# Performance work log

Measured on AMD Instinct MI355X. Metric: run time of the kernel, lower is better.

Reference implementation:

```python
import jax, jax.numpy as jnp
import numpy as np

DIM = 1024
INTER = 512
E = 16            # n_routed_experts
TOPK = 4          # n_activated_experts
N_GROUPS = 4
TOPK_GROUPS = 2
ROUTE_SCALE = 1.0
INIT_STD = 0.02
B, S = 2, 1024


def setup_inputs() -> dict:
    key = jax.random.key(0)
    ks = jax.random.split(key, 8)
    return {
        "x": jax.random.normal(ks[0], (B, S, DIM), jnp.float32),
        "gate_w": jax.random.normal(ks[1], (E, DIM), jnp.float32) * INIT_STD,
        "gate_bias": jnp.zeros((E,), jnp.float32),
        "w1": jax.random.normal(ks[2], (E, INTER, DIM), jnp.float32) * INIT_STD,
        "w2": jax.random.normal(ks[3], (E, DIM, INTER), jnp.float32) * INIT_STD,
        "w3": jax.random.normal(ks[4], (E, INTER, DIM), jnp.float32) * INIT_STD,
        "ws1": jax.random.normal(ks[5], (INTER, DIM), jnp.float32) * INIT_STD,
        "ws2": jax.random.normal(ks[6], (DIM, INTER), jnp.float32) * INIT_STD,
        "ws3": jax.random.normal(ks[7], (INTER, DIM), jnp.float32) * INIT_STD,
    }


def reference(x, gate_w, gate_bias, w1, w2, w3, ws1, ws2, ws3):
    Bx, Sx, D = x.shape
    T = Bx * Sx
    xf = x.reshape(T, D)

    # ---- Gate: sigmoid scores + expert bias, group-limited top-k ----
    scores = jax.nn.sigmoid(xf @ gate_w.T)          # [T, E]
    original_scores = scores
    s = scores + gate_bias                          # bias only affects selection
    sg = s.reshape(T, N_GROUPS, E // N_GROUPS)
    group_scores = sg.max(axis=-1)                  # [T, G]
    _, gidx = jax.lax.top_k(group_scores, TOPK_GROUPS)
    keep = jnp.zeros((T, N_GROUPS), bool).at[jnp.arange(T)[:, None], gidx].set(True)
    s_masked = jnp.where(keep[:, :, None], sg, -jnp.inf).reshape(T, E)
    _, idx = jax.lax.top_k(s_masked, TOPK)          # [T, topk]
    weights = jnp.take_along_axis(original_scores, idx, axis=1) * ROUTE_SCALE

    # combine weights as sparse [T, E] matrix (scatter of top-k weights)
    comb = jnp.zeros((T, E), x.dtype).at[jnp.arange(T)[:, None], idx].add(weights)

    # ---- Routed experts: SwiGLU per expert, weighted combine ----
    h1 = jnp.einsum('td,eid->tei', xf, w1)          # [T, E, inter]
    h3 = jnp.einsum('td,eid->tei', xf, w3)
    h = jax.nn.silu(h1) * h3
    y = jnp.einsum('tei,edi,te->td', h, w2, comb)   # weighted combine

    # ---- Shared expert (SwiGLU MLP) ----
    z = (jax.nn.silu(xf @ ws1.T) * (xf @ ws3.T)) @ ws2.T

    return (y + z).reshape(Bx, Sx, D)
```

## Files before the change

### kernel.cpp

```cpp
#include <hip/hip_runtime.h>

#define T_TOK  2048
#define DIMD   1024
#define INTERI 512
#define NEXP   16
#define NSEG   17

typedef __bf16 bf16x8 __attribute__((ext_vector_type(8)));
typedef float  f32x4  __attribute__((ext_vector_type(4)));

__device__ __forceinline__ unsigned short f2b(float f) {
    union { float f; unsigned int u; } c; c.f = f;
    unsigned int u = c.u;
    unsigned int r = (u + 0x7FFFu + ((u >> 16) & 1u)) >> 16;
    return (unsigned short)r;
}

__device__ __forceinline__ void cp16(const unsigned short* g, unsigned short* l) {
    __builtin_amdgcn_global_load_lds(
        (const __attribute__((address_space(1))) unsigned int*)g,
        (__attribute__((address_space(3))) unsigned int*)l,
        16, 0, 0);
}

__global__ __launch_bounds__(256) void cvt_all_kernel(
    const float* __restrict__ x,  const float* __restrict__ w1,
    const float* __restrict__ w3, const float* __restrict__ w2,
    const float* __restrict__ ws1, const float* __restrict__ ws3,
    const float* __restrict__ ws2,
    unsigned short* __restrict__ xb,  unsigned short* __restrict__ w1b,
    unsigned short* __restrict__ w3b, unsigned short* __restrict__ w2b,
    unsigned short* __restrict__ ws1b, unsigned short* __restrict__ ws3b,
    unsigned short* __restrict__ ws2b)
{
    int g = blockIdx.x * 256 + threadIdx.x;
    const float* s; unsigned short* d; int i;
    if      (g < 524288)  { s = x;   d = xb;   i = g; }
    else if (g < 2621440) { s = w1;  d = w1b;  i = g - 524288; }
    else if (g < 4718592) { s = w3;  d = w3b;  i = g - 2621440; }
    else if (g < 6815744) { s = w2;  d = w2b;  i = g - 4718592; }
    else if (g < 6946816) { s = ws1; d = ws1b; i = g - 6815744; }
    else if (g < 7077888) { s = ws3; d = ws3b; i = g - 6946816; }
    else                  { s = ws2; d = ws2b; i = g - 7077888; }
    float4 v = ((const float4*)s)[i];
    ushort4 o;
    o.x = f2b(v.x); o.y = f2b(v.y); o.z = f2b(v.z); o.w = f2b(v.w);
    ((ushort4*)d)[i] = o;
}

__global__ __launch_bounds__(256) void gate_score_kernel(
    const float* __restrict__ x, const float* __restrict__ gw,
    const float* __restrict__ gb,
    unsigned* __restrict__ sel, float4* __restrict__ selw)
{
    int tok  = blockIdx.x * 4 + (threadIdx.x >> 6);
    int lane = threadIdx.x & 63;
    const float* xp = x + (size_t)tok * DIMD;
    float xv[16];
#pragma unroll
    for (int j = 0; j < 16; ++j) xv[j] = xp[j * 64 + lane];

    float sc[16];
#pragma unroll
    for (int e = 0; e < 16; ++e) {
        const float* gwe = gw + e * DIMD;
        float p0 = 0.f, p1 = 0.f;
#pragma unroll
        for (int j = 0; j < 16; j += 2) {
            p0 += xv[j]     * gwe[j * 64 + lane];
            p1 += xv[j + 1] * gwe[(j + 1) * 64 + lane];
        }
        float p = p0 + p1;
#pragma unroll
        for (int o = 32; o; o >>= 1) p += __shfl_xor(p, o, 64);
        sc[e] = p;
    }
    if (lane != 0) return;

    float orig[16], s[16];
#pragma unroll
    for (int e = 0; e < 16; ++e) {
        orig[e] = 1.f / (1.f + expf(-sc[e]));
        s[e] = orig[e] + gb[e];
    }
    float gmax[4];
#pragma unroll
    for (int g = 0; g < 4; ++g) {
        float m = s[4 * g];
        for (int j = 1; j < 4; ++j) m = fmaxf(m, s[4 * g + j]);
        gmax[g] = m;
    }
    int g0 = 0;
    for (int g = 1; g < 4; ++g) if (gmax[g] > gmax[g0]) g0 = g;
    int g1 = -1;
    for (int g = 0; g < 4; ++g) { if (g == g0) continue; if (g1 < 0 || gmax[g] > gmax[g1]) g1 = g; }
    unsigned keep = (0xFu << (4 * g0)) | (0xFu << (4 * g1));
    unsigned used = 0;
    unsigned pk = 0;
    float w4[4];
    for (int j = 0; j < 4; ++j) {
        int best = -1;
        for (int e = 0; e < 16; ++e) {
            if (!((keep >> e) & 1u) || ((used >> e) & 1u)) continue;
            if (best < 0 || s[e] > s[best]) best = e;
        }
        used |= 1u << best;
        pk |= ((unsigned)best) << (4 * j);
        w4[j] = orig[best];
    }
    sel[tok] = pk;
    selw[tok] = make_float4(w4[0], w4[1], w4[2], w4[3]);
}

__global__ __launch_bounds__(256) void build_lists_kernel(
    const unsigned* __restrict__ sel, const float4* __restrict__ selw,
    int* __restrict__ counts, int* __restrict__ lst, float* __restrict__ lstw)
{
    const int e    = blockIdx.x;
    const int tid  = threadIdx.x;
    const int wave = tid >> 6;
    const int lane = tid & 63;

    __shared__ int wsum[4];
    __shared__ int basev;
    if (tid == 0) basev = 0;
    __syncthreads();

    for (int c = 0; c < T_TOK / 256; ++c) {
        int t = c * 256 + tid;
        unsigned s = sel[t];
        int match = -1;
#pragma unroll
        for (int j = 0; j < 4; ++j)
            if (((s >> (4 * j)) & 15u) == (unsigned)e) match = j;
        unsigned long long m = __ballot(match >= 0);
        int wpre = __popcll(m & ((1ull << lane) - 1ull));
        if (lane == 0) wsum[wave] = __popcll(m);
        __syncthreads();
        int pre = basev;
        for (int wv = 0; wv < wave; ++wv) pre += wsum[wv];
        if (match >= 0) {
            int pos = pre + wpre;
            lst [e * T_TOK + pos] = t | (match << 16);
            const float* wp = (const float*)&selw[t];
            lstw[e * T_TOK + pos] = wp[match];
        }
        __syncthreads();
        if (tid == 0) basev += wsum[0] + wsum[1] + wsum[2] + wsum[3];
        __syncthreads();
    }
    if (tid == 0) counts[e] = basev;
}

__global__ __launch_bounds__(256, 4) void gemm1_kernel(
    const unsigned short* __restrict__ xb,
    const unsigned short* __restrict__ w1b,
    const unsigned short* __restrict__ w3b,
    const unsigned short* __restrict__ ws1b,
    const unsigned short* __restrict__ ws3b,
    const int* __restrict__ counts,
    const int* __restrict__ lst,
    unsigned short* __restrict__ H)
{
    int b = blockIdx.x;
    int seg, mt, nt;
    if (b < 2048) {
        int xcd = b & 7, slot = b >> 3;
        seg = xcd + 8 * (slot >> 7);
        int tile = slot & 127;
        nt = tile & 3; mt = tile >> 2;
    } else {
        seg = NEXP;
        int tile = b - 2048;
        nt = tile & 3; mt = tile >> 2;
    }
    const int n_e = (seg == NEXP) ? T_TOK : counts[seg];
    const int m0  = mt * 64;
    if (m0 >= n_e) return;
    const int n0  = nt * 128;

    const unsigned short* w1p = (seg == NEXP) ? ws1b : w1b + (size_t)seg * INTERI * DIMD;
    const unsigned short* w3p = (seg == NEXP) ? ws3b : w3b + (size_t)seg * INTERI * DIMD;
    const int* lste = lst + seg * T_TOK;

    __shared__ __align__(16) unsigned short lA [2][64][32];
    __shared__ __align__(16) unsigned short lB1[2][128][32];
    __shared__ __align__(16) unsigned short lB3[2][128][32];

    const int tid  = threadIdx.x;
    const int wave = tid >> 6;
    const int lane = tid & 63;
    const int r4   = tid >> 2;
    const int skg  = (tid & 3) * 8;

    int ra = m0 + r4; if (ra > n_e - 1) ra = n_e - 1;
    int tok = (seg == NEXP) ? ra : (lste[ra] & 0xFFFF);
    const unsigned short* gA  = xb  + (size_t)tok * DIMD + skg;
    const unsigned short* gB1a = w1p + (size_t)(n0 + r4) * DIMD + skg;
    const unsigned short* gB1b = w1p + (size_t)(n0 + r4 + 64) * DIMD + skg;
    const unsigned short* gB3a = w3p + (size_t)(n0 + r4) * DIMD + skg;
    const unsigned short* gB3b = w3p + (size_t)(n0 + r4 + 64) * DIMD + skg;

    const int wb = wave * 512;

    f32x4 acc1[2][4], acc3[2][4];
    const f32x4 zero = {0.f, 0.f, 0.f, 0.f};
#pragma unroll
    for (int i = 0; i < 2; ++i)
#pragma unroll
        for (int j = 0; j < 4; ++j) { acc1[i][j] = zero; acc3[i][j] = zero; }

    const int wm   = (wave & 1) * 32;
    const int wn   = (wave >> 1) * 64;
    const int quad = lane >> 4;
    const int lrow = lane & 15;

    for (int k0 = 0; k0 < DIMD; k0 += 64) {
#pragma unroll
        for (int kk = 0; kk < 2; ++kk) {
            cp16(gA   + k0 + kk * 32, &lA [kk][0][0]  + wb);
            cp16(gB1a + k0 + kk * 32, &lB1[kk][0][0]  + wb);
            cp16(gB1b + k0 + kk * 32, &lB1[kk][64][0] + wb);
            cp16(gB3a + k0 + kk * 32, &lB3[kk][0][0]  + wb);
            cp16(gB3b + k0 + kk * 32, &lB3[kk][64][0] + wb);
        }
        __syncthreads();
#pragma unroll
        for (int kk = 0; kk < 2; ++kk) {
            bf16x8 a[2], b1[4], b3[4];
#pragma unroll
            for (int t = 0; t < 2; ++t)
                a[t] = *(const bf16x8*)&lA[kk][wm + t * 16 + lrow][quad * 8];
#pragma unroll
            for (int t = 0; t < 4; ++t) {
                b1[t] = *(const bf16x8*)&lB1[kk][wn + t * 16 + lrow][quad * 8];
                b3[t] = *(const bf16x8*)&lB3[kk][wn + t * 16 + lrow][quad * 8];
            }
#pragma unroll
            for (int i = 0; i < 2; ++i)
#pragma unroll
                for (int j = 0; j < 4; ++j) {
                    acc1[i][j] = __builtin_amdgcn_mfma_f32_16x16x32_bf16(a[i], b1[j], acc1[i][j], 0, 0, 0);
                    acc3[i][j] = __builtin_amdgcn_mfma_f32_16x16x32_bf16(a[i], b3[j], acc3[i][j], 0, 0, 0);
                }
        }
        __syncthreads();
    }

    unsigned short* Hseg = H + (size_t)seg * T_TOK * INTERI;
#pragma unroll
    for (int i = 0; i < 2; ++i) {
        int rbase = m0 + wm + i * 16 + quad * 4;
#pragma unroll
        for (int r = 0; r < 4; ++r) {
            int row = rbase + r;
            if (row >= n_e) continue;
            unsigned short* hrow = Hseg + (size_t)row * INTERI + n0 + wn + lrow;
#pragma unroll
            for (int j = 0; j < 4; ++j) {
                float v1 = acc1[i][j][r];
                float v3 = acc3[i][j][r];
                float hv = (v1 / (1.f + __expf(-v1))) * v3;
                hrow[j * 16] = f2b(hv);
            }
        }
    }
}

__global__ __launch_bounds__(256, 4) void gemm2_kernel(
    const unsigned short* __restrict__ H,
    const unsigned short* __restrict__ w2b,
    const unsigned short* __restrict__ ws2b,
    const int* __restrict__ counts,
    const int* __restrict__ lst,
    const float* __restrict__ lstw,
    float* __restrict__ P)
{
    int b = blockIdx.x;
    int seg, mt, nt;
    if (b < 4096) {
        int xcd = b & 7, slot = b >> 3;
        seg = xcd + 8 * (slot >> 8);
        int tile = slot & 255;
        nt = tile & 7; mt = tile >> 3;
    } else {
        seg = NEXP;
        int tile = b - 4096;
        nt = tile & 7; mt = tile >> 3;
    }
    const int n_e = (seg == NEXP) ? T_TOK : counts[seg];
    const int m0  = mt * 64;
    if (m0 >= n_e) return;
    const int n0  = nt * 128;

    const unsigned short* w2p  = (seg == NEXP) ? ws2b : w2b + (size_t)seg * DIMD * INTERI;
    const unsigned short* Hseg = H + (size_t)seg * T_TOK * INTERI;

    __shared__ __align__(16) unsigned short lA[2][64][32];
    __shared__ __align__(16) unsigned short lB[2][128][32];

    const int tid  = threadIdx.x;
    const int wave = tid >> 6;
    const int lane = tid & 63;
    const int r4   = tid >> 2;
    const int skg  = (tid & 3) * 8;

    int ra = m0 + r4; if (ra > n_e - 1) ra = n_e - 1;
    const unsigned short* gA  = Hseg + (size_t)ra * INTERI + skg;
    const unsigned short* gB0 = w2p + (size_t)(n0 + r4) * INTERI + skg;
    const unsigned short* gB1 = w2p + (size_t)(n0 + r4 + 64) * INTERI + skg;

    const int wb = wave * 512;

    f32x4 acc[2][4];
    const f32x4 zero = {0.f, 0.f, 0.f, 0.f};
#pragma unroll
    for (int i = 0; i < 2; ++i)
#pragma unroll
        for (int j = 0; j < 4; ++j) acc[i][j] = zero;

    const int wm   = (wave & 1) * 32;
    const int wn   = (wave >> 1) * 64;
    const int quad = lane >> 4;
    const int lrow = lane & 15;

    for (int k0 = 0; k0 < INTERI; k0 += 64) {
#pragma unroll
        for (int kk = 0; kk < 2; ++kk) {
            cp16(gA  + k0 + kk * 32, &lA[kk][0][0]  + wb);
            cp16(gB0 + k0 + kk * 32, &lB[kk][0][0]  + wb);
            cp16(gB1 + k0 + kk * 32, &lB[kk][64][0] + wb);
        }
        __syncthreads();
#pragma unroll
        for (int kk = 0; kk < 2; ++kk) {
            bf16x8 a[2], bv[4];
#pragma unroll
            for (int t = 0; t < 2; ++t)
                a[t] = *(const bf16x8*)&lA[kk][wm + t * 16 + lrow][quad * 8];
#pragma unroll
            for (int t = 0; t < 4; ++t)
                bv[t] = *(const bf16x8*)&lB[kk][wn + t * 16 + lrow][quad * 8];
#pragma unroll
            for (int i = 0; i < 2; ++i)
#pragma unroll
                for (int j = 0; j < 4; ++j)
                    acc[i][j] = __builtin_amdgcn_mfma_f32_16x16x32_bf16(a[i], bv[j], acc[i][j], 0, 0, 0);
        }
        __syncthreads();
    }

#pragma unroll
    for (int i = 0; i < 2; ++i) {
        int rbase = m0 + wm + i * 16 + quad * 4;
#pragma unroll
        for (int r = 0; r < 4; ++r) {
            int row = rbase + r;
            if (row >= n_e) continue;
            int tok, slot; float wt;
            if (seg == NEXP) { tok = row; slot = 4; wt = 1.f; }
            else {
                int ent = lst[seg * T_TOK + row];
                tok = ent & 0xFFFF; slot = ent >> 16;
                wt = lstw[seg * T_TOK + row];
            }
            float* prow = P + ((size_t)slot * T_TOK + tok) * DIMD + n0 + wn + lrow;
#pragma unroll
            for (int j = 0; j < 4; ++j)
                prow[j * 16] = wt * acc[i][j][r];
        }
    }
}

__global__ __launch_bounds__(256) void combine_kernel(
    const float4* __restrict__ P, float4* __restrict__ y)
{
    const int i = blockIdx.x * 256 + threadIdx.x;
    const size_t plane = (size_t)T_TOK * DIMD / 4;
    float4 a = P[i];
    float4 b = P[plane + i];
    float4 c = P[2 * plane + i];
    float4 d = P[3 * plane + i];
    float4 e = P[4 * plane + i];
    float4 o;
    o.x = a.x + b.x + c.x + d.x + e.x;
    o.y = a.y + b.y + c.y + d.y + e.y;
    o.z = a.z + b.z + c.z + d.z + e.z;
    o.w = a.w + b.w + c.w + d.w + e.w;
    y[i] = o;
}

extern "C" void kernel_launch(void* const* d_in, const int* in_sizes, int n_in,
                              void* d_out, int out_size, void* d_ws, size_t ws_size,
                              hipStream_t stream)
{
    const float* x   = (const float*)d_in[0];
    const float* gw  = (const float*)d_in[1];
    const float* gb  = (const float*)d_in[2];
    const float* w1  = (const float*)d_in[3];
    const float* w2  = (const float*)d_in[4];
    const float* w3  = (const float*)d_in[5];
    const float* ws1 = (const float*)d_in[6];
    const float* ws2 = (const float*)d_in[7];
    const float* ws3 = (const float*)d_in[8];

    char* base = (char*)d_ws;
    size_t off = 0;
    auto alloc = [&](size_t bytes) {
        char* q = base + off; off += (bytes + 255) & ~(size_t)255; return q;
    };
    unsigned short* xb   = (unsigned short*)alloc((size_t)T_TOK * DIMD * 2);
    unsigned short* w1b  = (unsigned short*)alloc((size_t)NEXP * INTERI * DIMD * 2);
    unsigned short* w3b  = (unsigned short*)alloc((size_t)NEXP * INTERI * DIMD * 2);
    unsigned short* w2b  = (unsigned short*)alloc((size_t)NEXP * DIMD * INTERI * 2);
    unsigned short* ws1b = (unsigned short*)alloc((size_t)INTERI * DIMD * 2);
    unsigned short* ws3b = (unsigned short*)alloc((size_t)INTERI * DIMD * 2);
    unsigned short* ws2b = (unsigned short*)alloc((size_t)DIMD * INTERI * 2);
    unsigned short* Hb   = (unsigned short*)alloc((size_t)NSEG * T_TOK * INTERI * 2);
    int*            cnts = (int*)alloc(NEXP * 4);
    int*            lstp = (int*)alloc((size_t)NEXP * T_TOK * 4);
    float*          lstw = (float*)alloc((size_t)NEXP * T_TOK * 4);
    unsigned*       selp = (unsigned*)alloc((size_t)T_TOK * 4);
    float4*         selw = (float4*)alloc((size_t)T_TOK * 16);
    float*          Pb   = (float*)alloc((size_t)5 * T_TOK * DIMD * 4);

    cvt_all_kernel<<<28160, 256, 0, stream>>>(x, w1, w3, w2, ws1, ws3, ws2,
                                              xb, w1b, w3b, w2b, ws1b, ws3b, ws2b);
    gate_score_kernel<<<T_TOK / 4, 256, 0, stream>>>(x, gw, gb, selp, selw);
    build_lists_kernel<<<NEXP, 256, 0, stream>>>(selp, selw, cnts, lstp, lstw);
    gemm1_kernel<<<2176, 256, 0, stream>>>(xb, w1b, w3b, ws1b, ws3b, cnts, lstp, Hb);
    gemm2_kernel<<<4352, 256, 0, stream>>>(Hb, w2b, ws2b, cnts, lstp, lstw, Pb);
    combine_kernel<<<(T_TOK * DIMD / 4) / 256, 256, 0, stream>>>((const float4*)Pb, (float4*)d_out);
}
```

Before: 257.9 us.

## Prefetch next K-tile into registers to overlap global loads with MFMA

Replaces direct global-to-LDS async copies in both expert GEMM kernels with register-staged loads. The next K-slice is loaded into registers while MFMAs run on the current LDS tile, then stored to LDS. Barriers become an explicit lgkmcnt wait plus s_barrier. This is meant to hide global load latency that the old load-then-sync pattern exposed each iteration. In exchange it uses more VGPRs for staging and adds LDS store instructions.

```diff
diff --git a/kernel.cpp b/kernel.cpp
--- a/kernel.cpp
+++ b/kernel.cpp
@@ -16,11 +16,9 @@
     return (unsigned short)r;
 }
 
-__device__ __forceinline__ void cp16(const unsigned short* g, unsigned short* l) {
-    __builtin_amdgcn_global_load_lds(
-        (const __attribute__((address_space(1))) unsigned int*)g,
-        (__attribute__((address_space(3))) unsigned int*)l,
-        16, 0, 0);
+__device__ __forceinline__ void lds_barrier() {
+    asm volatile("s_waitcnt lgkmcnt(0)" ::: "memory");
+    __builtin_amdgcn_s_barrier();
 }
 
 __global__ __launch_bounds__(256) void cvt_all_kernel(
@@ -195,13 +193,27 @@
 
     int ra = m0 + r4; if (ra > n_e - 1) ra = n_e - 1;
     int tok = (seg == NEXP) ? ra : (lste[ra] & 0xFFFF);
-    const unsigned short* gA  = xb  + (size_t)tok * DIMD + skg;
+    const unsigned short* gA   = xb  + (size_t)tok * DIMD + skg;
     const unsigned short* gB1a = w1p + (size_t)(n0 + r4) * DIMD + skg;
     const unsigned short* gB1b = w1p + (size_t)(n0 + r4 + 64) * DIMD + skg;
     const unsigned short* gB3a = w3p + (size_t)(n0 + r4) * DIMD + skg;
     const unsigned short* gB3b = w3p + (size_t)(n0 + r4 + 64) * DIMD + skg;
 
-    const int wb = wave * 512;
+    bf16x8 pa[2], pb1a[2], pb1b[2], pb3a[2], pb3b[2];
+
+#define G1LOAD(k0) do { _Pragma("unroll") for (int kk = 0; kk < 2; ++kk) { \
+    pa  [kk] = *(const bf16x8*)(gA   + (k0) + kk * 32); \
+    pb1a[kk] = *(const bf16x8*)(gB1a + (k0) + kk * 32); \
+    pb1b[kk] = *(const bf16x8*)(gB1b + (k0) + kk * 32); \
+    pb3a[kk] = *(const bf16x8*)(gB3a + (k0) + kk * 32); \
+    pb3b[kk] = *(const bf16x8*)(gB3b + (k0) + kk * 32); } } while (0)
+
+#define G1STORE() do { _Pragma("unroll") for (int kk = 0; kk < 2; ++kk) { \
+    *(bf16x8*)&lA [kk][r4][skg]      = pa  [kk]; \
+    *(bf16x8*)&lB1[kk][r4][skg]      = pb1a[kk]; \
+    *(bf16x8*)&lB1[kk][64 + r4][skg] = pb1b[kk]; \
+    *(bf16x8*)&lB3[kk][r4][skg]      = pb3a[kk]; \
+    *(bf16x8*)&lB3[kk][64 + r4][skg] = pb3b[kk]; } } while (0)
 
     f32x4 acc1[2][4], acc3[2][4];
     const f32x4 zero = {0.f, 0.f, 0.f, 0.f};
@@ -215,16 +227,12 @@
     const int quad = lane >> 4;
     const int lrow = lane & 15;
 
-    for (int k0 = 0; k0 < DIMD; k0 += 64) {
-#pragma unroll
-        for (int kk = 0; kk < 2; ++kk) {
-            cp16(gA   + k0 + kk * 32, &lA [kk][0][0]  + wb);
-            cp16(gB1a + k0 + kk * 32, &lB1[kk][0][0]  + wb);
-            cp16(gB1b + k0 + kk * 32, &lB1[kk][64][0] + wb);
-            cp16(gB3a + k0 + kk * 32, &lB3[kk][0][0]  + wb);
-            cp16(gB3b + k0 + kk * 32, &lB3[kk][64][0] + wb);
-        }
-        __syncthreads();
+    G1LOAD(0);
+    const int NK = DIMD / 64;
+    for (int it = 0; it < NK; ++it) {
+        G1STORE();
+        lds_barrier();
+        if (it + 1 < NK) G1LOAD((it + 1) * 64);
 #pragma unroll
         for (int kk = 0; kk < 2; ++kk) {
             bf16x8 a[2], b1[4], b3[4];
@@ -244,8 +252,10 @@
                     acc3[i][j] = __builtin_amdgcn_mfma_f32_16x16x32_bf16(a[i], b3[j], acc3[i][j], 0, 0, 0);
                 }
         }
-        __syncthreads();
-    }
+        lds_barrier();
+    }
+#undef G1LOAD
+#undef G1STORE
 
     unsigned short* Hseg = H + (size_t)seg * T_TOK * INTERI;
 #pragma unroll
@@ -310,7 +320,17 @@
     const unsigned short* gB0 = w2p + (size_t)(n0 + r4) * INTERI + skg;
     const unsigned short* gB1 = w2p + (size_t)(n0 + r4 + 64) * INTERI + skg;
 
-    const int wb = wave * 512;
+    bf16x8 pa[2], pb0[2], pb1[2];
+
+#define G2LOAD(k0) do { _Pragma("unroll") for (int kk = 0; kk < 2; ++kk) { \
+    pa [kk] = *(const bf16x8*)(gA  + (k0) + kk * 32); \
+    pb0[kk] = *(const bf16x8*)(gB0 + (k0) + kk * 32); \
+    pb1[kk] = *(const bf16x8*)(gB1 + (k0) + kk * 32); } } while (0)
+
+#define G2STORE() do { _Pragma("unroll") for (int kk = 0; kk < 2; ++kk) { \
+    *(bf16x8*)&lA[kk][r4][skg]      = pa [kk]; \
+    *(bf16x8*)&lB[kk][r4][skg]      = pb0[kk]; \
+    *(bf16x8*)&lB[kk][64 + r4][skg] = pb1[kk]; } } while (0)
 
     f32x4 acc[2][4];
     const f32x4 zero = {0.f, 0.f, 0.f, 0.f};
@@ -324,14 +344,12 @@
     const int quad = lane >> 4;
     const int lrow = lane & 15;
 
-    for (int k0 = 0; k0 < INTERI; k0 += 64) {
-#pragma unroll
-        for (int kk = 0; kk < 2; ++kk) {
-            cp16(gA  + k0 + kk * 32, &lA[kk][0][0]  + wb);
-            cp16(gB0 + k0 + kk * 32, &lB[kk][0][0]  + wb);
-            cp16(gB1 + k0 + kk * 32, &lB[kk][64][0] + wb);
-        }
-        __syncthreads();
+    G2LOAD(0);
+    const int NK = INTERI / 64;
+    for (int it = 0; it < NK; ++it) {
+        G2STORE();
+        lds_barrier();
+        if (it + 1 < NK) G2LOAD((it + 1) * 64);
 #pragma unroll
         for (int kk = 0; kk < 2; ++kk) {
             bf16x8 a[2], bv[4];
@@ -347,8 +365,10 @@
                 for (int j = 0; j < 4; ++j)
                     acc[i][j] = __builtin_amdgcn_mfma_f32_16x16x32_bf16(a[i], bv[j], acc[i][j], 0, 0, 0);
         }
-        __syncthreads();
-    }
+        lds_barrier();
+    }
+#undef G2LOAD
+#undef G2STORE
 
 #pragma unroll
     for (int i = 0; i < 2; ++i) {
```

Measured after the change: 257.8 us. About the same (-0.0%).
